# Optimization experiments

Hardware: AMD Instinct MI355X
Metric: run time of the kernel (lower is better)

The kernel has to match this reference:

```python
import jax, jax.numpy as jnp
import numpy as np

WH, WW = 16, 16
NUM_HEADS = 16
DIM = 1024
BATCH = 64
SEQ = WH * WW + 1  # 257, includes cls token
NUM_REL = (2 * WH - 1) * (2 * WW - 1) + 3  # 964


def _make_rel_pos_index(wh, ww):
    # BEiT relative position index construction (intended semantics of the torch code)
    coords = np.stack(np.meshgrid(np.arange(wh), np.arange(ww), indexing='ij'))  # [2, wh, ww]
    flat = coords.reshape(2, -1)  # [2, wh*ww]
    rel = flat[:, :, None] - flat[:, None, :]  # [2, N-1, N-1]
    rel = rel.transpose(1, 2, 0).astype(np.int64)
    rel[:, :, 0] += wh - 1
    rel[:, :, 1] += ww - 1
    rel[:, :, 0] *= 2 * ww - 1
    num_rel = (2 * wh - 1) * (2 * ww - 1) + 3
    idx = np.zeros((wh * ww + 1, wh * ww + 1), dtype=np.int32)
    idx[1:, 1:] = rel.sum(-1)
    idx[0, :] = num_rel - 3  # cls-to-token
    idx[:, 0] = num_rel - 2  # token-to-cls
    idx[0, 0] = num_rel - 1  # cls-to-cls
    return idx


def setup_inputs() -> dict:
    key = jax.random.key(0)
    ks = jax.random.split(key, 7)
    return {
        'x': jax.random.normal(ks[0], (BATCH, SEQ, DIM), dtype=jnp.float32),
        'qkv_weight': jax.random.normal(ks[1], (3 * DIM, DIM), dtype=jnp.float32) * 0.02,
        'query_bias': jax.random.normal(ks[2], (DIM,), dtype=jnp.float32) * 0.02,
        'value_bias': jax.random.normal(ks[3], (DIM,), dtype=jnp.float32) * 0.02,
        'rel_pos_bias_table': jax.random.normal(ks[4], (NUM_REL, NUM_HEADS), dtype=jnp.float32) * 0.02,
        'proj_weight': jax.random.normal(ks[5], (DIM, DIM), dtype=jnp.float32) * 0.02,
        'proj_bias': jax.random.normal(ks[6], (DIM,), dtype=jnp.float32) * 0.02,
        'rel_pos_index': jnp.asarray(_make_rel_pos_index(WH, WW)),
    }


def reference(x, qkv_weight, query_bias, value_bias, rel_pos_bias_table,
              proj_weight, proj_bias, rel_pos_index):
    B, N, C = x.shape
    H = rel_pos_bias_table.shape[-1]
    D = qkv_weight.shape[0] // 3 // H
    scale = D ** -0.5
    # qkv bias: (q_bias, zeros, v_bias) as in the torch module
    qkv_bias = jnp.concatenate([query_bias, jnp.zeros_like(value_bias), value_bias])
    qkv = x @ qkv_weight.T + qkv_bias  # [B, N, 3*H*D]
    qkv = qkv.reshape(B, N, 3, H, D).transpose(2, 0, 3, 1, 4)  # [3, B, H, N, D]
    q, k, v = qkv[0] * scale, qkv[1], qkv[2]
    attn = jnp.einsum('bhqd,bhkd->bhqk', q, k)  # [B, H, N, N]
    bias = rel_pos_bias_table[rel_pos_index]  # [N, N, H]
    attn = attn + bias.transpose(2, 0, 1)[None]  # add per-head bias
    attn = jax.nn.softmax(attn, axis=-1)
    out = jnp.einsum('bhqk,bhkd->bhqd', attn, v)  # [B, H, N, D]
    out = out.transpose(0, 2, 1, 3).reshape(B, N, H * D)
    return out @ proj_weight.T + proj_bias
```

## Files before the change

### kernel.cpp

```cpp
#include <hip/hip_runtime.h>


typedef unsigned short u16;
typedef __attribute__((ext_vector_type(8))) short bf16x8;
typedef __attribute__((ext_vector_type(4))) float f32x4;

#define MFMA16(a, b, c) __builtin_amdgcn_mfma_f32_16x16x32_bf16(a, b, c, 0, 0, 0)
#define GLDS16(g, l)                                                           \
  __builtin_amdgcn_global_load_lds(                                            \
      (const __attribute__((address_space(1))) void*)(g),                      \
      (__attribute__((address_space(3))) void*)(l), 16, 0, 0)

#define QOFF 0
#define KOFF 16842752
#define VTOFF 33685504
#define VTP 264

__device__ __forceinline__ u16 f2bf(float f) {
  unsigned u = __builtin_bit_cast(unsigned, f);
  u += 0x7FFFu + ((u >> 16) & 1u);
  return (u16)(u >> 16);
}
__device__ __forceinline__ unsigned pack2(float a, float b) {
  return (unsigned)f2bf(a) | ((unsigned)f2bf(b) << 16);
}

__global__ __launch_bounds__(256) void cvt_bf16(const float* __restrict__ in,
                                                u16* __restrict__ out, int n4) {
  int i = blockIdx.x * 256 + threadIdx.x;
  if (i < n4) {
    float4 v = ((const float4*)in)[i];
    uint2 o;
    o.x = pack2(v.x, v.y);
    o.y = pack2(v.z, v.w);
    ((uint2*)out)[i] = o;
  }
}

__global__ __launch_bounds__(256) void bias_pre(const float* __restrict__ tab,
                                                const int* __restrict__ idx,
                                                float* __restrict__ out) {
  int t = blockIdx.x * 256 + threadIdx.x;
  if (t < 66049) {
    int id = idx[t];
    const float* row = tab + (size_t)id * 16;
#pragma unroll
    for (int h = 0; h < 16; h++)
      out[(size_t)h * 66049 + t] = row[h] * 1.4426950408889634f;
  }
}


#define GEMM_PROLOG(M_, K_)                                                    \
  __shared__ __align__(16) u16 As[128 * 32];                                   \
  __shared__ __align__(16) u16 Bs[128 * 32];                                   \
  const int M = (M_), K = (K_);                                                \
  const int tid = threadIdx.x;                                                 \
  const int lane = tid & 63, wave = tid >> 6;                                  \
  const int quad = lane >> 4, l15 = lane & 15;                                 \
  const int wr = (wave >> 1) * 64, wc = (wave & 1) * 64;                       \
  const int m0 = blockIdx.y * 128, n0 = blockIdx.x * 128;                      \
  const int sgk = (((tid & 3) ^ ((tid >> 3) & 3))) * 8;  \
  const int fo = ((quad ^ ((l15 >> 1) & 3))) * 8;         \
  int ar0 = m0 + (tid >> 2); if (ar0 > M - 1) ar0 = M - 1;                     \
  int ar1 = m0 + 64 + (tid >> 2); if (ar1 > M - 1) ar1 = M - 1;                \
  const u16* pa0 = A + (size_t)ar0 * K + sgk;                                  \
  const u16* pa1 = A + (size_t)ar1 * K + sgk;                                  \
  const u16* pb0 = B + (size_t)(n0 + (tid >> 2)) * K + sgk;                    \
  const u16* pb1 = pb0 + (size_t)64 * K;                                       \
  f32x4 acc[4][4];                                                             \
  _Pragma("unroll") for (int i = 0; i < 4; i++)                                \
  _Pragma("unroll") for (int j = 0; j < 4; j++)                                \
      acc[i][j] = (f32x4){0.f, 0.f, 0.f, 0.f};                                 \
  for (int k0 = 0; k0 < K; k0 += 32) {                                         \
    __syncthreads();                                                           \
    GLDS16(pa0 + k0, As + tid * 8);                                            \
    GLDS16(pa1 + k0, As + 2048 + tid * 8);                                     \
    GLDS16(pb0 + k0, Bs + tid * 8);                                            \
    GLDS16(pb1 + k0, Bs + 2048 + tid * 8);                                     \
    __syncthreads();                                                           \
    bf16x8 af[4], bf[4];                                                       \
    _Pragma("unroll") for (int t = 0; t < 4; t++)                              \
        af[t] = *(const bf16x8*)(As + (wr + t * 16 + l15) * 32 + fo);          \
    _Pragma("unroll") for (int t = 0; t < 4; t++)                              \
        bf[t] = *(const bf16x8*)(Bs + (wc + t * 16 + l15) * 32 + fo);          \
    _Pragma("unroll") for (int i = 0; i < 4; i++)                              \
    _Pragma("unroll") for (int j = 0; j < 4; j++)                              \
        acc[i][j] = MFMA16(af[i], bf[j], acc[i][j]);                           \
  }

__global__ __launch_bounds__(256) void gemm_qkv(
    const u16* __restrict__ A, const u16* __restrict__ B,
    const float* __restrict__ qbias, const float* __restrict__ vbias,
    u16* __restrict__ C) {
  GEMM_PROLOG(16448, 1024)
#pragma unroll
  for (int i = 0; i < 4; i++) {
#pragma unroll
    for (int r = 0; r < 4; r++) {
      int row = m0 + wr + i * 16 + quad * 4 + r;
      if (row < M) {
        unsigned bb = (unsigned)row / 257u;
        unsigned nn = (unsigned)row - bb * 257u;
#pragma unroll
        for (int j = 0; j < 4; j++) {
          int c = n0 + wc + j * 16 + l15;
          int which = c >> 10, rem = c & 1023;
          float bias = (which == 0) ? qbias[rem]
                                    : ((which == 2) ? vbias[rem] : 0.f);
          float v = acc[i][j][r] + bias;
          if (which == 0) v *= 0.18033688011112042f;
          int h = rem >> 6, d = rem & 63;
          size_t dst;
          if (which == 2) {
            dst = (size_t)VTOFF + ((size_t)(bb * 16 + h) * 64 + d) * VTP + nn;
          } else {
            dst = (size_t)which * 16842752 + (size_t)(bb * 16 + h) * 16448 +
                  (size_t)nn * 64 + d;
          }
          C[dst] = f2bf(v);
        }
      }
    }
  }
}

__global__ __launch_bounds__(256) void gemm_proj(
    const u16* __restrict__ A, const u16* __restrict__ B,
    const float* __restrict__ pbias, float* __restrict__ C) {
  GEMM_PROLOG(16448, 1024)
#pragma unroll
  for (int i = 0; i < 4; i++) {
#pragma unroll
    for (int r = 0; r < 4; r++) {
      int row = m0 + wr + i * 16 + quad * 4 + r;
      if (row < M) {
#pragma unroll
        for (int j = 0; j < 4; j++) {
          int c = n0 + wc + j * 16 + l15;
          C[(size_t)row * 1024 + c] = acc[i][j][r] + pbias[c];
        }
      }
    }
  }
}

__global__ __launch_bounds__(256, 3) void attn_fused(
    const u16* __restrict__ qkv, const float* __restrict__ biasT,
    u16* __restrict__ out) {
  __shared__ __align__(16) u16 KVs[96 * 72];
  __shared__ __align__(16) u16 Ps[4 * 16 * 104];
  const int bx = blockIdx.x;
  const int qt = bx % 5, bh = bx / 5;
  const int b = bh >> 4, h = bh & 15;
  const int tid = threadIdx.x, lane = tid & 63, wave = tid >> 6;
  const int quad = lane >> 4, l15 = lane & 15;
  const u16* qg = qkv + QOFF + (size_t)bh * 16448;
  const u16* kg = qkv + KOFF + (size_t)bh * 16448;
  const u16* vtg = qkv + VTOFF + (size_t)bh * (64 * VTP);

  int qra = qt * 64 + wave * 16 + l15;
  if (qra > 256) qra = 256;
  const bf16x8 aq0 = *(const bf16x8*)(qg + (size_t)qra * 64 + quad * 8);
  const bf16x8 aq1 = *(const bf16x8*)(qg + (size_t)qra * 64 + 32 + quad * 8);

  const int qbase = qt * 64 + wave * 16 + quad * 4;
  const float* bb = biasT + (size_t)h * 66049;
  f32x4 s[18];
#pragma unroll
  for (int r = 0; r < 4; r++) {
    int qr = qbase + r;
    if (qr > 256) qr = 256;
    const float* brow = bb + (size_t)qr * 257;
#pragma unroll
    for (int t = 0; t < 18; t++) {
      int kc = t * 16 + l15;
      s[t][r] = (kc < 257) ? brow[kc] : -3e38f;
    }
  }

  const bf16x8 zv = {0, 0, 0, 0, 0, 0, 0, 0};
  for (int ck = 0; ck < 3; ck++) {
    __syncthreads();
#pragma unroll
    for (int it = 0; it < 3; it++) {
      int g = it * 256 + tid;
      int row = g >> 3, col = (g & 7) * 8;
      int gr = ck * 96 + row;
      bf16x8 kv = (gr < 257) ? *(const bf16x8*)(kg + (size_t)gr * 64 + col) : zv;
      *(bf16x8*)(KVs + row * 72 + col) = kv;
    }
    __syncthreads();
#pragma unroll
    for (int nt = 0; nt < 6; nt++) {
      bf16x8 b0 = *(const bf16x8*)(KVs + (nt * 16 + l15) * 72 + quad * 8);
      bf16x8 b1 = *(const bf16x8*)(KVs + (nt * 16 + l15) * 72 + 32 + quad * 8);
      int t = ck * 6 + nt;
      s[t] = MFMA16(aq0, b0, s[t]);
      s[t] = MFMA16(aq1, b1, s[t]);
    }
  }

  float inv[4];
#pragma unroll
  for (int r = 0; r < 4; r++) {
    float m = -3e38f;
#pragma unroll
    for (int t = 0; t < 18; t++) m = fmaxf(m, s[t][r]);
    m = fmaxf(m, __shfl_xor(m, 1));
    m = fmaxf(m, __shfl_xor(m, 2));
    m = fmaxf(m, __shfl_xor(m, 4));
    m = fmaxf(m, __shfl_xor(m, 8));
    float sum = 0.f;
#pragma unroll
    for (int t = 0; t < 18; t++) {
      float p = __builtin_amdgcn_exp2f(s[t][r] - m);
      s[t][r] = p;
      sum += p;
    }
    sum += __shfl_xor(sum, 1);
    sum += __shfl_xor(sum, 2);
    sum += __shfl_xor(sum, 4);
    sum += __shfl_xor(sum, 8);
    inv[r] = 1.f / sum;
  }

  u16* Pw = Ps + wave * (16 * 104);
  f32x4 o[4];
#pragma unroll
  for (int nt = 0; nt < 4; nt++) o[nt] = (f32x4){0.f, 0.f, 0.f, 0.f};
  for (int ck = 0; ck < 3; ck++) {
    __syncthreads();
#pragma unroll
    for (int it = 0; it < 3; it++) {
      int g = it * 256 + tid;
      int row = g / 12, c = (g % 12) * 8;
      bf16x8 v = *(const bf16x8*)(vtg + (size_t)row * VTP + ck * 96 + c);
      *(bf16x8*)(KVs + row * 104 + c) = v;
    }
#pragma unroll
    for (int nt = 0; nt < 6; nt++) {
      int t = ck * 6 + nt;
#pragma unroll
      for (int r = 0; r < 4; r++)
        Pw[(quad * 4 + r) * 104 + nt * 16 + l15] = f2bf(s[t][r]);
    }
    __syncthreads();
#pragma unroll
    for (int ks = 0; ks < 3; ks++) {
      bf16x8 ap = *(const bf16x8*)(Pw + l15 * 104 + ks * 32 + quad * 8);
#pragma unroll
      for (int nt = 0; nt < 4; nt++) {
        bf16x8 bv =
            *(const bf16x8*)(KVs + (nt * 16 + l15) * 104 + ks * 32 + quad * 8);
        o[nt] = MFMA16(ap, bv, o[nt]);
      }
    }
  }

#pragma unroll
  for (int nt = 0; nt < 4; nt++) {
    int d = nt * 16 + l15;
#pragma unroll
    for (int r = 0; r < 4; r++) {
      int qr = qbase + r;
      if (qr < 257)
        out[((size_t)b * 257 + qr) * 1024 + h * 64 + d] =
            f2bf(o[nt][r] * inv[r]);
    }
  }
}

extern "C" void kernel_launch(void* const* d_in, const int* in_sizes, int n_in,
                              void* d_out, int out_size, void* d_ws,
                              size_t ws_size, hipStream_t stream) {
  const float* x = (const float*)d_in[0];
  const float* qkvw = (const float*)d_in[1];
  const float* qb = (const float*)d_in[2];
  const float* vb = (const float*)d_in[3];
  const float* tab = (const float*)d_in[4];
  const float* pw = (const float*)d_in[5];
  const float* pb = (const float*)d_in[6];
  const int* rpi = (const int*)d_in[7];

  char* ws = (char*)d_ws;
  u16* qkvbuf = (u16*)ws;
  u16* xbuf = (u16*)(ws + 101974016);
  float* biasb = (float*)(ws + 135659520);
  u16* qkvwb = (u16*)(ws + 139886656);
  u16* projwb = (u16*)(ws + 146178112);

  cvt_bf16<<<16448, 256, 0, stream>>>(x, xbuf, 4210688);
  cvt_bf16<<<3072, 256, 0, stream>>>(qkvw, qkvwb, 786432);
  cvt_bf16<<<1024, 256, 0, stream>>>(pw, projwb, 262144);
  bias_pre<<<259, 256, 0, stream>>>(tab, rpi, biasb);
  gemm_qkv<<<dim3(24, 129), 256, 0, stream>>>(xbuf, qkvwb, qb, vb, qkvbuf);
  attn_fused<<<5120, 256, 0, stream>>>(qkvbuf, biasb, xbuf);
  gemm_proj<<<dim3(8, 129), 256, 0, stream>>>(xbuf, projwb, pb, (float*)d_out);
}
```

Measured before the change: 467.3 us.

## Double-buffer GEMM LDS tiles and remap blocks for XCD-local reuse

The GEMM main loop now uses two LDS buffers per operand and prefetches the next K-slice with global_load_lds while MFMAs run on the current one. This drops one barrier per iteration and is meant to hide global load latency. Both GEMMs and the attention kernel now use a 1D grid with a block-index remap, so blocks landing on the same XCD (index mod 8) share the same weight column tiles or the same batch-head rows, which should improve L2 reuse. Doubling the LDS footprint may lower occupancy.

```diff
diff --git a/kernel.cpp b/kernel.cpp
--- a/kernel.cpp
+++ b/kernel.cpp
@@ -51,15 +51,18 @@
 }
 
 
-#define GEMM_PROLOG(M_, K_)                                                    \
-  __shared__ __align__(16) u16 As[128 * 32];                                   \
-  __shared__ __align__(16) u16 Bs[128 * 32];                                   \
+#define GEMM_PROLOG(M_, K_, W_)                                                \
+  __shared__ __align__(16) u16 As[2][4096];                                    \
+  __shared__ __align__(16) u16 Bs[2][4096];                                    \
   const int M = (M_), K = (K_);                                                \
   const int tid = threadIdx.x;                                                 \
   const int lane = tid & 63, wave = tid >> 6;                                  \
   const int quad = lane >> 4, l15 = lane & 15;                                 \
   const int wr = (wave >> 1) * 64, wc = (wave & 1) * 64;                       \
-  const int m0 = blockIdx.y * 128, n0 = blockIdx.x * 128;                      \
+  const int lid = blockIdx.x;                                                  \
+  const int xcd8 = lid & 7, li = lid >> 3;                                     \
+  const int m0 = (li / (W_)) * 128;                                            \
+  const int n0 = (xcd8 * (W_) + li % (W_)) * 128;                              \
   const int sgk = (((tid & 3) ^ ((tid >> 3) & 3))) * 8;  \
   const int fo = ((quad ^ ((l15 >> 1) & 3))) * 8;         \
   int ar0 = m0 + (tid >> 2); if (ar0 > M - 1) ar0 = M - 1;                     \
@@ -72,28 +75,36 @@
   _Pragma("unroll") for (int i = 0; i < 4; i++)                                \
   _Pragma("unroll") for (int j = 0; j < 4; j++)                                \
       acc[i][j] = (f32x4){0.f, 0.f, 0.f, 0.f};                                 \
+  GLDS16(pa0, &As[0][tid * 8]);                                                \
+  GLDS16(pa1, &As[0][2048 + tid * 8]);                                         \
+  GLDS16(pb0, &Bs[0][tid * 8]);                                                \
+  GLDS16(pb1, &Bs[0][2048 + tid * 8]);                                         \
+  __syncthreads();                                                             \
+  int cur = 0;                                                                 \
   for (int k0 = 0; k0 < K; k0 += 32) {                                         \
-    __syncthreads();                                                           \
-    GLDS16(pa0 + k0, As + tid * 8);                                            \
-    GLDS16(pa1 + k0, As + 2048 + tid * 8);                                     \
-    GLDS16(pb0 + k0, Bs + tid * 8);                                            \
-    GLDS16(pb1 + k0, Bs + 2048 + tid * 8);                                     \
-    __syncthreads();                                                           \
+    if (k0 + 32 < K) {             \
+      GLDS16(pa0 + k0 + 32, &As[cur ^ 1][tid * 8]);                            \
+      GLDS16(pa1 + k0 + 32, &As[cur ^ 1][2048 + tid * 8]);                     \
+      GLDS16(pb0 + k0 + 32, &Bs[cur ^ 1][tid * 8]);                            \
+      GLDS16(pb1 + k0 + 32, &Bs[cur ^ 1][2048 + tid * 8]);                     \
+    }                                                                          \
     bf16x8 af[4], bf[4];                                                       \
     _Pragma("unroll") for (int t = 0; t < 4; t++)                              \
-        af[t] = *(const bf16x8*)(As + (wr + t * 16 + l15) * 32 + fo);          \
+        af[t] = *(const bf16x8*)(&As[cur][(wr + t * 16 + l15) * 32 + fo]);     \
     _Pragma("unroll") for (int t = 0; t < 4; t++)                              \
-        bf[t] = *(const bf16x8*)(Bs + (wc + t * 16 + l15) * 32 + fo);          \
+        bf[t] = *(const bf16x8*)(&Bs[cur][(wc + t * 16 + l15) * 32 + fo]);     \
     _Pragma("unroll") for (int i = 0; i < 4; i++)                              \
     _Pragma("unroll") for (int j = 0; j < 4; j++)                              \
         acc[i][j] = MFMA16(af[i], bf[j], acc[i][j]);                           \
+    __syncthreads();    \
+    cur ^= 1;                                                                  \
   }
 
 __global__ __launch_bounds__(256) void gemm_qkv(
     const u16* __restrict__ A, const u16* __restrict__ B,
     const float* __restrict__ qbias, const float* __restrict__ vbias,
     u16* __restrict__ C) {
-  GEMM_PROLOG(16448, 1024)
+  GEMM_PROLOG(16448, 1024, 3)
 #pragma unroll
   for (int i = 0; i < 4; i++) {
 #pragma unroll
@@ -128,7 +139,7 @@
 __global__ __launch_bounds__(256) void gemm_proj(
     const u16* __restrict__ A, const u16* __restrict__ B,
     const float* __restrict__ pbias, float* __restrict__ C) {
-  GEMM_PROLOG(16448, 1024)
+  GEMM_PROLOG(16448, 1024, 1)
 #pragma unroll
   for (int i = 0; i < 4; i++) {
 #pragma unroll
@@ -151,7 +162,9 @@
   __shared__ __align__(16) u16 KVs[96 * 72];
   __shared__ __align__(16) u16 Ps[4 * 16 * 104];
   const int bx = blockIdx.x;
-  const int qt = bx % 5, bh = bx / 5;
+  const int xj = bx & 7, xi = bx >> 3;
+  const int qt = xi % 5;
+  const int bh = (xi / 5) * 8 + xj;
   const int b = bh >> 4, h = bh & 15;
   const int tid = threadIdx.x, lane = tid & 63, wave = tid >> 6;
   const int quad = lane >> 4, l15 = lane & 15;
@@ -294,7 +307,7 @@
   cvt_bf16<<<3072, 256, 0, stream>>>(qkvw, qkvwb, 786432);
   cvt_bf16<<<1024, 256, 0, stream>>>(pw, projwb, 262144);
   bias_pre<<<259, 256, 0, stream>>>(tab, rpi, biasb);
-  gemm_qkv<<<dim3(24, 129), 256, 0, stream>>>(xbuf, qkvwb, qb, vb, qkvbuf);
+  gemm_qkv<<<3096, 256, 0, stream>>>(xbuf, qkvwb, qb, vb, qkvbuf);
   attn_fused<<<5120, 256, 0, stream>>>(qkvbuf, biasb, xbuf);
-  gemm_proj<<<dim3(8, 129), 256, 0, stream>>>(xbuf, projwb, pb, (float*)d_out);
-}
+  gemm_proj<<<1032, 256, 0, stream>>>(xbuf, projwb, pb, (float*)d_out);
+}
```

Measured after the change: 566.5 us. +21.2%, slower.
